# Optimization experiments

Hardware: AMD Instinct MI355X
Metric: run time of the kernel (lower is better)

The kernel has to match this reference:

```python
import jax, jax.numpy as jnp
import numpy as np

N = 100000
E = 1600000
G = 2048          # number of graphs in the batch
HEADS = 4
HID = 16          # per-head channels
IN_CH = 128
D = HEADS * HID   # 64, concat output width per layer
NEG_SLOPE = 0.2


def _gat_layer(x, src, dst, W, a_src, a_dst, bias):
    # x: [N, Fin], W: [Fin, H*C], a_src/a_dst: [H, C], bias: [H*C]
    h = (x @ W).reshape(N, HEADS, HID)                      # [N, H, C]
    al_s = jnp.einsum('nhc,hc->nh', h, a_src)               # [N, H]
    al_d = jnp.einsum('nhc,hc->nh', h, a_dst)               # [N, H]
    e = jax.nn.leaky_relu(al_s[src] + al_d[dst], NEG_SLOPE) # [E+N, H]
    # segment softmax over incoming edges of each destination node
    m = jax.ops.segment_max(e, dst, num_segments=N)         # [N, H]
    e = jnp.exp(e - m[dst])
    s = jax.ops.segment_sum(e, dst, num_segments=N)
    alpha = e / (s[dst] + 1e-16)                            # [E+N, H]
    msg = h[src] * alpha[..., None]                         # [E+N, H, C]
    out = jax.ops.segment_sum(msg, dst, num_segments=N)     # [N, H, C]
    return out.reshape(N, D) + bias


def setup_inputs() -> dict:
    key = jax.random.key(0)
    ks = jax.random.split(key, 16)
    x = jax.random.normal(ks[0], (N, IN_CH), dtype=jnp.float32)
    edge_index = jax.random.randint(ks[1], (2, E), 0, N, dtype=jnp.int64)
    batch = jnp.sort(jax.random.randint(ks[2], (N,), 0, G, dtype=jnp.int64))
    inp = {'x': x, 'edge_index': edge_index, 'batch': batch}
    fins = [IN_CH, D, D]
    for i, fin in enumerate(fins):
        kk = jax.random.split(ks[3 + i], 4)
        sc = 1.0 / np.sqrt(fin)
        inp[f'W{i}'] = jax.random.normal(kk[0], (fin, D), dtype=jnp.float32) * sc
        inp[f'as{i}'] = jax.random.normal(kk[1], (HEADS, HID), dtype=jnp.float32) * 0.1
        inp[f'ad{i}'] = jax.random.normal(kk[2], (HEADS, HID), dtype=jnp.float32) * 0.1
        inp[f'b{i}'] = jnp.zeros((D,), dtype=jnp.float32)
    inp['head_w'] = jax.random.normal(ks[10], (1, D), dtype=jnp.float32) * (1.0 / np.sqrt(D))
    inp['head_b'] = jnp.zeros((1,), dtype=jnp.float32)
    return inp


def reference(x, edge_index, batch,
              W0, as0, ad0, b0,
              W1, as1, ad1, b1,
              W2, as2, ad2, b2,
              head_w, head_b):
    # PyG GATConv adds self-loops by default
    loops = jnp.arange(N, dtype=edge_index.dtype)
    src = jnp.concatenate([edge_index[0], loops])
    dst = jnp.concatenate([edge_index[1], loops])
    layers = [(W0, as0, ad0, b0), (W1, as1, ad1, b1), (W2, as2, ad2, b2)]
    h = x.astype(jnp.float32)
    for (W, a_s, a_d, b) in layers:
        h = _gat_layer(h, src, dst, W, a_s, a_d, b)
        h = jax.nn.relu(h)  # dropout p=0.0 -> identity
    pooled = jax.ops.segment_sum(h, batch, num_segments=G)  # [G, D]
    out = pooled @ head_w.T + head_b                         # [G, 1]
    return out.reshape(-1)                                   # out_dim == 1 -> flatten
```

## Files before the change

### kernel.cpp

```cpp
#include <hip/hip_runtime.h>
#include <hip/hip_bf16.h>
#include <hip/hip_fp16.h>
#include <cstdint>
#include <cstddef>

#define NN 100000
#define EE 1600000
#define GG 2048

constexpr int NB_SCAN = (NN + 255) / 256;

__device__ __forceinline__ float lrelu(float v) { return v > 0.f ? v : 0.2f * v; }

__global__ void k_count(const int* __restrict__ ei, int* __restrict__ deg,
                        int* __restrict__ rank) {
    int i = blockIdx.x * blockDim.x + threadIdx.x;
    if (i >= EE + NN) return;
    int d = (i < EE) ? ei[EE + i] : (i - EE);
    rank[i] = atomicAdd(&deg[d], 1);
}

__global__ void k_scan1(const int* __restrict__ deg, int* __restrict__ offs,
                        int* __restrict__ bsums) {
    __shared__ int tmp[256];
    int tid = threadIdx.x;
    int i = blockIdx.x * 256 + tid;
    int v = (i < NN) ? deg[i] : 0;
    tmp[tid] = v; __syncthreads();
    for (int off = 1; off < 256; off <<= 1) {
        int t = (tid >= off) ? tmp[tid - off] : 0;
        __syncthreads();
        tmp[tid] += t;
        __syncthreads();
    }
    if (i < NN) offs[i] = tmp[tid] - v;
    if (tid == 255) bsums[blockIdx.x] = tmp[255];
}

__global__ void k_scan2(int* __restrict__ bsums) {
    __shared__ int tmp[512];
    int tid = threadIdx.x;
    int v = (tid < NB_SCAN) ? bsums[tid] : 0;
    tmp[tid] = v; __syncthreads();
    for (int off = 1; off < 512; off <<= 1) {
        int t = (tid >= off) ? tmp[tid - off] : 0;
        __syncthreads();
        tmp[tid] += t;
        __syncthreads();
    }
    if (tid < NB_SCAN) bsums[tid] = tmp[tid] - v;
}

__global__ void k_scan3(int* __restrict__ offs, const int* __restrict__ bsums) {
    int i = blockIdx.x * 256 + threadIdx.x;
    if (i < NN) offs[i] += bsums[blockIdx.x];
}

__global__ void k_scatter(const int* __restrict__ ei, const int* __restrict__ offs,
                          const int* __restrict__ rank, int* __restrict__ col) {
    int i = blockIdx.x * blockDim.x + threadIdx.x;
    if (i >= EE + NN) return;
    int s, d;
    if (i < EE) { s = ei[i]; d = ei[EE + i]; } else { s = d = i - EE; }
    col[offs[d] + rank[i]] = s;
}

template <int FIN>
__global__ __launch_bounds__(256) void k_gemm(const float* __restrict__ X,
                                              const float* __restrict__ W,
                                              const float* __restrict__ asrc,
                                              const float* __restrict__ adst,
                                              float* __restrict__ H,
                                              float* __restrict__ als,
                                              float* __restrict__ ald) {
    int j  = threadIdx.x & 63;
    int ty = threadIdx.x >> 6;
    int row = __builtin_amdgcn_readfirstlane(blockIdx.x * 16 + ty * 4);
    const float* x0 = X + (size_t)row * FIN;
    const float* x1 = x0 + FIN;
    const float* x2 = x1 + FIN;
    const float* x3 = x2 + FIN;
    float a0 = 0.f, a1 = 0.f, a2 = 0.f, a3 = 0.f;
#pragma unroll
    for (int k = 0; k < FIN; k += 4) {
        float4 xa = *(const float4*)(x0 + k);
        float4 xb = *(const float4*)(x1 + k);
        float4 xc = *(const float4*)(x2 + k);
        float4 xd = *(const float4*)(x3 + k);
        float w0 = W[(k + 0) * 64 + j];
        float w1 = W[(k + 1) * 64 + j];
        float w2 = W[(k + 2) * 64 + j];
        float w3 = W[(k + 3) * 64 + j];
        a0 += xa.x * w0 + xa.y * w1 + xa.z * w2 + xa.w * w3;
        a1 += xb.x * w0 + xb.y * w1 + xb.z * w2 + xb.w * w3;
        a2 += xc.x * w0 + xc.y * w1 + xc.z * w2 + xc.w * w3;
        a3 += xd.x * w0 + xd.y * w1 + xd.z * w2 + xd.w * w3;
    }
    H[(size_t)(row + 0) * 64 + j] = a0;
    H[(size_t)(row + 1) * 64 + j] = a1;
    H[(size_t)(row + 2) * 64 + j] = a2;
    H[(size_t)(row + 3) * 64 + j] = a3;
    float asj = asrc[j], adj = adst[j];
    float accs[4] = {a0, a1, a2, a3};
#pragma unroll
    for (int r = 0; r < 4; r++) {
        float vs = accs[r] * asj;
        float vd = accs[r] * adj;
#pragma unroll
        for (int off = 8; off > 0; off >>= 1) {
            vs += __shfl_xor(vs, off, 64);
            vd += __shfl_xor(vd, off, 64);
        }
        if ((j & 15) == 0) {
            int h = j >> 4;
            als[(size_t)(row + r) * 4 + h] = vs;
            ald[(size_t)(row + r) * 4 + h] = vd;
        }
    }
}

#define LWPITCH 260
__global__ __launch_bounds__(256) void k_agg(
    const float* __restrict__ H, const float* __restrict__ als,
    const float* __restrict__ ald, const int* __restrict__ offs,
    const int* __restrict__ deg, const int* __restrict__ col,
    const float* __restrict__ bias, float* __restrict__ Hout,
    const int* __restrict__ batch, const float* __restrict__ hw,
    float* __restrict__ out, int last) {
    __shared__ float lws[16 * LWPITCH];
    __shared__ int   lsi[16][64];
    int tid = threadIdx.x;
    int g = tid >> 4;
    int l = tid & 15;
    int n = blockIdx.x * 16 + g;
    int start = offs[n];
    int len = deg[n];
    float4 ad4 = ((const float4*)ald)[n];
    int hsel = l >> 2;
    const float4* Hp = (const float4*)H + l;
    float* lw = lws + g * LWPITCH;
    bool fast = (len <= 64);
    float inv = 1.f;

    if (fast) {
        float ev[4][4];
        int   si[4];
        bool  vld[4];
        float m0 = -1e30f, m1 = -1e30f, m2 = -1e30f, m3 = -1e30f;
#pragma unroll
        for (int it = 0; it < 4; it++) {
            int e = l + it * 16;
            vld[it] = (e < len);
            int s = vld[it] ? col[start + e] : 0;
            si[it] = s;
            float4 a = ((const float4*)als)[s];
            ev[it][0] = lrelu(a.x + ad4.x); ev[it][1] = lrelu(a.y + ad4.y);
            ev[it][2] = lrelu(a.z + ad4.z); ev[it][3] = lrelu(a.w + ad4.w);
            if (vld[it]) {
                m0 = fmaxf(m0, ev[it][0]); m1 = fmaxf(m1, ev[it][1]);
                m2 = fmaxf(m2, ev[it][2]); m3 = fmaxf(m3, ev[it][3]);
            }
        }
#pragma unroll
        for (int off = 8; off > 0; off >>= 1) {
            m0 = fmaxf(m0, __shfl_xor(m0, off, 16));
            m1 = fmaxf(m1, __shfl_xor(m1, off, 16));
            m2 = fmaxf(m2, __shfl_xor(m2, off, 16));
            m3 = fmaxf(m3, __shfl_xor(m3, off, 16));
        }
        float s0 = 0.f, s1 = 0.f, s2 = 0.f, s3 = 0.f;
#pragma unroll
        for (int it = 0; it < 4; it++) {
            int e = l + it * 16;
            float w0 = vld[it] ? __expf(ev[it][0] - m0) : 0.f;
            float w1 = vld[it] ? __expf(ev[it][1] - m1) : 0.f;
            float w2 = vld[it] ? __expf(ev[it][2] - m2) : 0.f;
            float w3 = vld[it] ? __expf(ev[it][3] - m3) : 0.f;
            s0 += w0; s1 += w1; s2 += w2; s3 += w3;
            ((float4*)(lw + e * 4))[0] = make_float4(w0, w1, w2, w3);
            lsi[g][e] = vld[it] ? si[it] : 0;
        }
#pragma unroll
        for (int off = 8; off > 0; off >>= 1) {
            s0 += __shfl_xor(s0, off, 16); s1 += __shfl_xor(s1, off, 16);
            s2 += __shfl_xor(s2, off, 16); s3 += __shfl_xor(s3, off, 16);
        }
        float smh = hsel == 0 ? s0 : hsel == 1 ? s1 : hsel == 2 ? s2 : s3;
        inv = 1.f / (smh + 1e-16f);
    }

    __syncthreads();

    float4 acc = {0.f, 0.f, 0.f, 0.f};
    if (fast) {
        int e = 0;
        for (; e + 4 <= len; e += 4) {
            int sa = lsi[g][e], sb = lsi[g][e + 1], sc = lsi[g][e + 2], sd = lsi[g][e + 3];
            float wa = lw[(e + 0) * 4 + hsel];
            float wb = lw[(e + 1) * 4 + hsel];
            float wc = lw[(e + 2) * 4 + hsel];
            float wd = lw[(e + 3) * 4 + hsel];
            float4 ha = Hp[(size_t)sa * 16];
            float4 hb = Hp[(size_t)sb * 16];
            float4 hc = Hp[(size_t)sc * 16];
            float4 hd = Hp[(size_t)sd * 16];
            acc.x += wa * ha.x + wb * hb.x + wc * hc.x + wd * hd.x;
            acc.y += wa * ha.y + wb * hb.y + wc * hc.y + wd * hd.y;
            acc.z += wa * ha.z + wb * hb.z + wc * hc.z + wd * hd.z;
            acc.w += wa * ha.w + wb * hb.w + wc * hc.w + wd * hd.w;
        }
        for (; e < len; e++) {
            int sa = lsi[g][e];
            float wa = lw[e * 4 + hsel];
            float4 ha = Hp[(size_t)sa * 16];
            acc.x += wa * ha.x; acc.y += wa * ha.y;
            acc.z += wa * ha.z; acc.w += wa * ha.w;
        }
    } else {
        float m0 = -1e30f, m1 = -1e30f, m2 = -1e30f, m3 = -1e30f;
        for (int e = l; e < len; e += 16) {
            int s = col[start + e];
            float4 a = ((const float4*)als)[s];
            m0 = fmaxf(m0, lrelu(a.x + ad4.x)); m1 = fmaxf(m1, lrelu(a.y + ad4.y));
            m2 = fmaxf(m2, lrelu(a.z + ad4.z)); m3 = fmaxf(m3, lrelu(a.w + ad4.w));
        }
#pragma unroll
        for (int off = 8; off > 0; off >>= 1) {
            m0 = fmaxf(m0, __shfl_xor(m0, off, 16));
            m1 = fmaxf(m1, __shfl_xor(m1, off, 16));
            m2 = fmaxf(m2, __shfl_xor(m2, off, 16));
            m3 = fmaxf(m3, __shfl_xor(m3, off, 16));
        }
        float s0 = 0.f, s1 = 0.f, s2 = 0.f, s3 = 0.f;
        for (int e = l; e < len; e += 16) {
            int s = col[start + e];
            float4 a = ((const float4*)als)[s];
            s0 += __expf(lrelu(a.x + ad4.x) - m0); s1 += __expf(lrelu(a.y + ad4.y) - m1);
            s2 += __expf(lrelu(a.z + ad4.z) - m2); s3 += __expf(lrelu(a.w + ad4.w) - m3);
        }
#pragma unroll
        for (int off = 8; off > 0; off >>= 1) {
            s0 += __shfl_xor(s0, off, 16); s1 += __shfl_xor(s1, off, 16);
            s2 += __shfl_xor(s2, off, 16); s3 += __shfl_xor(s3, off, 16);
        }
        float mh = hsel == 0 ? m0 : hsel == 1 ? m1 : hsel == 2 ? m2 : m3;
        float sh = hsel == 0 ? s0 : hsel == 1 ? s1 : hsel == 2 ? s2 : s3;
        float ih = 1.f / (sh + 1e-16f);
        float ah = hsel == 0 ? ad4.x : hsel == 1 ? ad4.y : hsel == 2 ? ad4.z : ad4.w;
        for (int e = 0; e < len; e++) {
            int s = col[start + e];
            float alpha = __expf(lrelu(als[(size_t)s * 4 + hsel] + ah) - mh) * ih;
            float4 ha = Hp[(size_t)s * 16];
            acc.x += alpha * ha.x; acc.y += alpha * ha.y;
            acc.z += alpha * ha.z; acc.w += alpha * ha.w;
        }
        inv = 1.f;
    }

    float4 b4 = ((const float4*)bias)[l];
    float4 o4;
    o4.x = fmaxf(acc.x * inv + b4.x, 0.f);
    o4.y = fmaxf(acc.y * inv + b4.y, 0.f);
    o4.z = fmaxf(acc.z * inv + b4.z, 0.f);
    o4.w = fmaxf(acc.w * inv + b4.w, 0.f);
    if (!last) {
        ((float4*)Hout)[(size_t)n * 16 + l] = o4;
    } else {
        float4 w4 = ((const float4*)hw)[l];
        float t = o4.x * w4.x + o4.y * w4.y + o4.z * w4.z + o4.w * w4.w;
#pragma unroll
        for (int off = 8; off > 0; off >>= 1) t += __shfl_xor(t, off, 16);
        if (l == 0) atomicAdd(&out[batch[n]], t);
    }
}

__global__ void k_out_init(const float* __restrict__ head_b, float* __restrict__ out) {
    int g = blockIdx.x * blockDim.x + threadIdx.x;
    if (g < GG) out[g] = head_b[0];
}

extern "C" void kernel_launch(void* const* d_in, const int* in_sizes, int n_in,
                              void* d_out, int out_size, void* d_ws, size_t ws_size,
                              hipStream_t stream) {
    const float* x     = (const float*)d_in[0];
    const int*   ei    = (const int*)d_in[1];
    const int*   batch = (const int*)d_in[2];
    const float* Wm[3] = {(const float*)d_in[3], (const float*)d_in[7],  (const float*)d_in[11]};
    const float* As[3] = {(const float*)d_in[4], (const float*)d_in[8],  (const float*)d_in[12]};
    const float* Ad[3] = {(const float*)d_in[5], (const float*)d_in[9],  (const float*)d_in[13]};
    const float* Bb[3] = {(const float*)d_in[6], (const float*)d_in[10], (const float*)d_in[14]};
    const float* hw = (const float*)d_in[15];
    const float* hb = (const float*)d_in[16];
    float* out = (float*)d_out;

    uint8_t* w = (uint8_t*)d_ws;
    auto alloc = [&](size_t bytes) -> void* {
        void* p = (void*)w;
        w += (bytes + 255) & ~(size_t)255;
        return p;
    };
    float* H       = (float*)alloc((size_t)NN * 64 * 4);
    float* Bf      = (float*)alloc((size_t)NN * 64 * 4);
    float* als     = (float*)alloc((size_t)NN * 4 * 4);
    float* ald     = (float*)alloc((size_t)NN * 4 * 4);
    int*   deg     = (int*)alloc((size_t)NN * 4);
    int*   offs    = (int*)alloc((size_t)NN * 4);
    int*   rank    = (int*)alloc((size_t)(EE + NN) * 4);
    int*   col     = (int*)alloc((size_t)(EE + NN) * 4);
    int*   bsums   = (int*)alloc((size_t)((NB_SCAN + 63) & ~63) * 4);

    hipMemsetAsync(deg, 0, (size_t)NN * 4, stream);

    int eb = (EE + NN + 255) / 256;
    k_count  <<<eb, 256, 0, stream>>>(ei, deg, rank);
    k_scan1  <<<NB_SCAN, 256, 0, stream>>>(deg, offs, bsums);
    k_scan2  <<<1, 512, 0, stream>>>(bsums);
    k_scan3  <<<NB_SCAN, 256, 0, stream>>>(offs, bsums);
    k_scatter<<<eb, 256, 0, stream>>>(ei, offs, rank, col);
    k_out_init<<<(GG + 255) / 256, 256, 0, stream>>>(hb, out);

    const float* cur_in = x;
    for (int L = 0; L < 3; L++) {
        if (L == 0)
            k_gemm<128><<<NN / 16, 256, 0, stream>>>(
                cur_in, Wm[L], As[L], Ad[L], H, als, ald);
        else
            k_gemm<64><<<NN / 16, 256, 0, stream>>>(
                cur_in, Wm[L], As[L], Ad[L], H, als, ald);
        k_agg <<<NN / 16, 256, 0, stream>>>(
            H, als, ald, offs, deg, col, Bb[L], Bf, batch, hw, out, (L == 2) ? 1 : 0);
        cur_in = Bf;
    }
}
```

Measured before the change: 540.5 us.

## Split aggregation into alpha pass and channel-sliced gather over planar H

The fused per-node aggregation is replaced by two kernels. The first computes normalized attention weights per edge and head into a head-major buffer. The second gathers from a feature matrix stored as 8 planes of 8 channels, so each pass touches a smaller, more cache-resident slice of H. Pooling moves to a separate kernel after the last layer. This adds an extra edge-sized alpha write and read per layer and re-reads the column indices 8 times, in exchange for better L2 locality in the gathers.

```diff
diff --git a/kernel.cpp b/kernel.cpp
--- a/kernel.cpp
+++ b/kernel.cpp
@@ -1,12 +1,12 @@
 #include <hip/hip_runtime.h>
 #include <hip/hip_bf16.h>
-#include <hip/hip_fp16.h>
 #include <cstdint>
 #include <cstddef>
 
 #define NN 100000
 #define EE 1600000
 #define GG 2048
+#define EN (EE + NN)
 
 constexpr int NB_SCAN = (NN + 255) / 256;
 
@@ -15,7 +15,7 @@
 __global__ void k_count(const int* __restrict__ ei, int* __restrict__ deg,
                         int* __restrict__ rank) {
     int i = blockIdx.x * blockDim.x + threadIdx.x;
-    if (i >= EE + NN) return;
+    if (i >= EN) return;
     int d = (i < EE) ? ei[EE + i] : (i - EE);
     rank[i] = atomicAdd(&deg[d], 1);
 }
@@ -59,7 +59,7 @@
 __global__ void k_scatter(const int* __restrict__ ei, const int* __restrict__ offs,
                           const int* __restrict__ rank, int* __restrict__ col) {
     int i = blockIdx.x * blockDim.x + threadIdx.x;
-    if (i >= EE + NN) return;
+    if (i >= EN) return;
     int s, d;
     if (i < EE) { s = ei[i]; d = ei[EE + i]; } else { s = d = i - EE; }
     col[offs[d] + rank[i]] = s;
@@ -70,7 +70,7 @@
                                               const float* __restrict__ W,
                                               const float* __restrict__ asrc,
                                               const float* __restrict__ adst,
-                                              float* __restrict__ H,
+                                              float* __restrict__ Hs,
                                               float* __restrict__ als,
                                               float* __restrict__ ald) {
     int j  = threadIdx.x & 63;
@@ -96,10 +96,9 @@
         a2 += xc.x * w0 + xc.y * w1 + xc.z * w2 + xc.w * w3;
         a3 += xd.x * w0 + xd.y * w1 + xd.z * w2 + xd.w * w3;
     }
-    H[(size_t)(row + 0) * 64 + j] = a0;
-    H[(size_t)(row + 1) * 64 + j] = a1;
-    H[(size_t)(row + 2) * 64 + j] = a2;
-    H[(size_t)(row + 3) * 64 + j] = a3;
+    int plane = j >> 3, cc = j & 7;
+    float* pb = Hs + ((size_t)plane * NN + row) * 8 + cc;
+    pb[0 * 8] = a0; pb[1 * 8] = a1; pb[2 * 8] = a2; pb[3 * 8] = a3;
     float asj = asrc[j], adj = adst[j];
     float accs[4] = {a0, a1, a2, a3};
 #pragma unroll
@@ -119,32 +118,19 @@
     }
 }
 
-#define LWPITCH 260
-__global__ __launch_bounds__(256) void k_agg(
-    const float* __restrict__ H, const float* __restrict__ als,
-    const float* __restrict__ ald, const int* __restrict__ offs,
-    const int* __restrict__ deg, const int* __restrict__ col,
-    const float* __restrict__ bias, float* __restrict__ Hout,
-    const int* __restrict__ batch, const float* __restrict__ hw,
-    float* __restrict__ out, int last) {
-    __shared__ float lws[16 * LWPITCH];
-    __shared__ int   lsi[16][64];
+__global__ __launch_bounds__(256) void k_alpha(
+    const float* __restrict__ als, const float* __restrict__ ald,
+    const int* __restrict__ offs, const int* __restrict__ deg,
+    const int* __restrict__ col, float* __restrict__ alpha) {
     int tid = threadIdx.x;
-    int g = tid >> 4;
-    int l = tid & 15;
+    int g = tid >> 4, l = tid & 15;
     int n = blockIdx.x * 16 + g;
     int start = offs[n];
     int len = deg[n];
     float4 ad4 = ((const float4*)ald)[n];
-    int hsel = l >> 2;
-    const float4* Hp = (const float4*)H + l;
-    float* lw = lws + g * LWPITCH;
-    bool fast = (len <= 64);
-    float inv = 1.f;
-
-    if (fast) {
+
+    if (len <= 64) {
         float ev[4][4];
-        int   si[4];
         bool  vld[4];
         float m0 = -1e30f, m1 = -1e30f, m2 = -1e30f, m3 = -1e30f;
 #pragma unroll
@@ -152,7 +138,6 @@
             int e = l + it * 16;
             vld[it] = (e < len);
             int s = vld[it] ? col[start + e] : 0;
-            si[it] = s;
             float4 a = ((const float4*)als)[s];
             ev[it][0] = lrelu(a.x + ad4.x); ev[it][1] = lrelu(a.y + ad4.y);
             ev[it][2] = lrelu(a.z + ad4.z); ev[it][3] = lrelu(a.w + ad4.w);
@@ -168,53 +153,32 @@
             m2 = fmaxf(m2, __shfl_xor(m2, off, 16));
             m3 = fmaxf(m3, __shfl_xor(m3, off, 16));
         }
+        float w[4][4];
         float s0 = 0.f, s1 = 0.f, s2 = 0.f, s3 = 0.f;
+#pragma unroll
+        for (int it = 0; it < 4; it++) {
+            w[it][0] = vld[it] ? __expf(ev[it][0] - m0) : 0.f;
+            w[it][1] = vld[it] ? __expf(ev[it][1] - m1) : 0.f;
+            w[it][2] = vld[it] ? __expf(ev[it][2] - m2) : 0.f;
+            w[it][3] = vld[it] ? __expf(ev[it][3] - m3) : 0.f;
+            s0 += w[it][0]; s1 += w[it][1]; s2 += w[it][2]; s3 += w[it][3];
+        }
+#pragma unroll
+        for (int off = 8; off > 0; off >>= 1) {
+            s0 += __shfl_xor(s0, off, 16); s1 += __shfl_xor(s1, off, 16);
+            s2 += __shfl_xor(s2, off, 16); s3 += __shfl_xor(s3, off, 16);
+        }
+        float i0 = 1.f / (s0 + 1e-16f), i1 = 1.f / (s1 + 1e-16f);
+        float i2 = 1.f / (s2 + 1e-16f), i3 = 1.f / (s3 + 1e-16f);
 #pragma unroll
         for (int it = 0; it < 4; it++) {
             int e = l + it * 16;
-            float w0 = vld[it] ? __expf(ev[it][0] - m0) : 0.f;
-            float w1 = vld[it] ? __expf(ev[it][1] - m1) : 0.f;
-            float w2 = vld[it] ? __expf(ev[it][2] - m2) : 0.f;
-            float w3 = vld[it] ? __expf(ev[it][3] - m3) : 0.f;
-            s0 += w0; s1 += w1; s2 += w2; s3 += w3;
-            ((float4*)(lw + e * 4))[0] = make_float4(w0, w1, w2, w3);
-            lsi[g][e] = vld[it] ? si[it] : 0;
-        }
-#pragma unroll
-        for (int off = 8; off > 0; off >>= 1) {
-            s0 += __shfl_xor(s0, off, 16); s1 += __shfl_xor(s1, off, 16);
-            s2 += __shfl_xor(s2, off, 16); s3 += __shfl_xor(s3, off, 16);
-        }
-        float smh = hsel == 0 ? s0 : hsel == 1 ? s1 : hsel == 2 ? s2 : s3;
-        inv = 1.f / (smh + 1e-16f);
-    }
-
-    __syncthreads();
-
-    float4 acc = {0.f, 0.f, 0.f, 0.f};
-    if (fast) {
-        int e = 0;
-        for (; e + 4 <= len; e += 4) {
-            int sa = lsi[g][e], sb = lsi[g][e + 1], sc = lsi[g][e + 2], sd = lsi[g][e + 3];
-            float wa = lw[(e + 0) * 4 + hsel];
-            float wb = lw[(e + 1) * 4 + hsel];
-            float wc = lw[(e + 2) * 4 + hsel];
-            float wd = lw[(e + 3) * 4 + hsel];
-            float4 ha = Hp[(size_t)sa * 16];
-            float4 hb = Hp[(size_t)sb * 16];
-            float4 hc = Hp[(size_t)sc * 16];
-            float4 hd = Hp[(size_t)sd * 16];
-            acc.x += wa * ha.x + wb * hb.x + wc * hc.x + wd * hd.x;
-            acc.y += wa * ha.y + wb * hb.y + wc * hc.y + wd * hd.y;
-            acc.z += wa * ha.z + wb * hb.z + wc * hc.z + wd * hd.z;
-            acc.w += wa * ha.w + wb * hb.w + wc * hc.w + wd * hd.w;
-        }
-        for (; e < len; e++) {
-            int sa = lsi[g][e];
-            float wa = lw[e * 4 + hsel];
-            float4 ha = Hp[(size_t)sa * 16];
-            acc.x += wa * ha.x; acc.y += wa * ha.y;
-            acc.z += wa * ha.z; acc.w += wa * ha.w;
+            if (vld[it]) {
+                alpha[0 * (size_t)EN + start + e] = w[it][0] * i0;
+                alpha[1 * (size_t)EN + start + e] = w[it][1] * i1;
+                alpha[2 * (size_t)EN + start + e] = w[it][2] * i2;
+                alpha[3 * (size_t)EN + start + e] = w[it][3] * i3;
+            }
         }
     } else {
         float m0 = -1e30f, m1 = -1e30f, m2 = -1e30f, m3 = -1e30f;
@@ -243,40 +207,85 @@
             s0 += __shfl_xor(s0, off, 16); s1 += __shfl_xor(s1, off, 16);
             s2 += __shfl_xor(s2, off, 16); s3 += __shfl_xor(s3, off, 16);
         }
-        float mh = hsel == 0 ? m0 : hsel == 1 ? m1 : hsel == 2 ? m2 : m3;
-        float sh = hsel == 0 ? s0 : hsel == 1 ? s1 : hsel == 2 ? s2 : s3;
-        float ih = 1.f / (sh + 1e-16f);
-        float ah = hsel == 0 ? ad4.x : hsel == 1 ? ad4.y : hsel == 2 ? ad4.z : ad4.w;
-        for (int e = 0; e < len; e++) {
+        float i0 = 1.f / (s0 + 1e-16f), i1 = 1.f / (s1 + 1e-16f);
+        float i2 = 1.f / (s2 + 1e-16f), i3 = 1.f / (s3 + 1e-16f);
+        for (int e = l; e < len; e += 16) {
             int s = col[start + e];
-            float alpha = __expf(lrelu(als[(size_t)s * 4 + hsel] + ah) - mh) * ih;
-            float4 ha = Hp[(size_t)s * 16];
-            acc.x += alpha * ha.x; acc.y += alpha * ha.y;
-            acc.z += alpha * ha.z; acc.w += alpha * ha.w;
-        }
-        inv = 1.f;
-    }
-
-    float4 b4 = ((const float4*)bias)[l];
+            float4 a = ((const float4*)als)[s];
+            alpha[0 * (size_t)EN + start + e] = __expf(lrelu(a.x + ad4.x) - m0) * i0;
+            alpha[1 * (size_t)EN + start + e] = __expf(lrelu(a.y + ad4.y) - m1) * i1;
+            alpha[2 * (size_t)EN + start + e] = __expf(lrelu(a.z + ad4.z) - m2) * i2;
+            alpha[3 * (size_t)EN + start + e] = __expf(lrelu(a.w + ad4.w) - m3) * i3;
+        }
+    }
+}
+
+__global__ __launch_bounds__(256) void k_slice(
+    const float* __restrict__ Hs, const float* __restrict__ alpha,
+    const int* __restrict__ offs, const int* __restrict__ deg,
+    const int* __restrict__ col, const float* __restrict__ bias,
+    float* __restrict__ Hout) {
+    int s = blockIdx.x & 7;
+    int t = blockIdx.x >> 3;
+    int n = t * 128 + (threadIdx.x >> 1);
+    if (n >= NN) return;
+    int c  = threadIdx.x & 1;
+    int c4 = s * 2 + c;
+    int h  = c4 >> 2;
+    const float*  ap = alpha + (size_t)h * EN;
+    const float4* Hp = (const float4*)Hs + (size_t)s * NN * 2 + c;
+    int start = offs[n];
+    int len = deg[n];
+    const int*   cp  = col + start;
+    const float* app = ap + start;
+    float4 acc = {0.f, 0.f, 0.f, 0.f};
+    int e = 0;
+    for (; e + 4 <= len; e += 4) {
+        int i0 = cp[e], i1 = cp[e + 1], i2 = cp[e + 2], i3 = cp[e + 3];
+        float a0 = app[e], a1 = app[e + 1], a2 = app[e + 2], a3 = app[e + 3];
+        float4 h0 = Hp[(size_t)i0 * 2];
+        float4 h1 = Hp[(size_t)i1 * 2];
+        float4 h2 = Hp[(size_t)i2 * 2];
+        float4 h3 = Hp[(size_t)i3 * 2];
+        acc.x += a0 * h0.x + a1 * h1.x + a2 * h2.x + a3 * h3.x;
+        acc.y += a0 * h0.y + a1 * h1.y + a2 * h2.y + a3 * h3.y;
+        acc.z += a0 * h0.z + a1 * h1.z + a2 * h2.z + a3 * h3.z;
+        acc.w += a0 * h0.w + a1 * h1.w + a2 * h2.w + a3 * h3.w;
+    }
+    for (; e < len; e++) {
+        int i0 = cp[e];
+        float a0 = app[e];
+        float4 h0 = Hp[(size_t)i0 * 2];
+        acc.x += a0 * h0.x; acc.y += a0 * h0.y;
+        acc.z += a0 * h0.z; acc.w += a0 * h0.w;
+    }
+    float4 b4 = ((const float4*)bias)[c4];
     float4 o4;
-    o4.x = fmaxf(acc.x * inv + b4.x, 0.f);
-    o4.y = fmaxf(acc.y * inv + b4.y, 0.f);
-    o4.z = fmaxf(acc.z * inv + b4.z, 0.f);
-    o4.w = fmaxf(acc.w * inv + b4.w, 0.f);
-    if (!last) {
-        ((float4*)Hout)[(size_t)n * 16 + l] = o4;
-    } else {
-        float4 w4 = ((const float4*)hw)[l];
-        float t = o4.x * w4.x + o4.y * w4.y + o4.z * w4.z + o4.w * w4.w;
-#pragma unroll
-        for (int off = 8; off > 0; off >>= 1) t += __shfl_xor(t, off, 16);
-        if (l == 0) atomicAdd(&out[batch[n]], t);
-    }
+    o4.x = fmaxf(acc.x + b4.x, 0.f);
+    o4.y = fmaxf(acc.y + b4.y, 0.f);
+    o4.z = fmaxf(acc.z + b4.z, 0.f);
+    o4.w = fmaxf(acc.w + b4.w, 0.f);
+    ((float4*)Hout)[(size_t)n * 16 + c4] = o4;
 }
 
 __global__ void k_out_init(const float* __restrict__ head_b, float* __restrict__ out) {
     int g = blockIdx.x * blockDim.x + threadIdx.x;
     if (g < GG) out[g] = head_b[0];
+}
+
+__global__ void k_pool(const float* __restrict__ H, const int* __restrict__ batch,
+                       const float* __restrict__ hw, float* __restrict__ out) {
+    int n = blockIdx.x * blockDim.x + threadIdx.x;
+    if (n >= NN) return;
+    const float4* hp = (const float4*)(H + (size_t)n * 64);
+    const float4* wp = (const float4*)hw;
+    float t = 0.f;
+#pragma unroll
+    for (int k = 0; k < 16; k++) {
+        float4 a = hp[k]; float4 b = wp[k];
+        t += a.x * b.x + a.y * b.y + a.z * b.z + a.w * b.w;
+    }
+    atomicAdd(&out[batch[n]], t);
 }
 
 extern "C" void kernel_launch(void* const* d_in, const int* in_sizes, int n_in,
@@ -299,19 +308,20 @@
         w += (bytes + 255) & ~(size_t)255;
         return p;
     };
-    float* H       = (float*)alloc((size_t)NN * 64 * 4);
-    float* Bf      = (float*)alloc((size_t)NN * 64 * 4);
-    float* als     = (float*)alloc((size_t)NN * 4 * 4);
-    float* ald     = (float*)alloc((size_t)NN * 4 * 4);
-    int*   deg     = (int*)alloc((size_t)NN * 4);
-    int*   offs    = (int*)alloc((size_t)NN * 4);
-    int*   rank    = (int*)alloc((size_t)(EE + NN) * 4);
-    int*   col     = (int*)alloc((size_t)(EE + NN) * 4);
-    int*   bsums   = (int*)alloc((size_t)((NB_SCAN + 63) & ~63) * 4);
+    float* Hs    = (float*)alloc((size_t)8 * NN * 8 * 4);
+    float* Bf    = (float*)alloc((size_t)NN * 64 * 4);
+    float* als   = (float*)alloc((size_t)NN * 4 * 4);
+    float* ald   = (float*)alloc((size_t)NN * 4 * 4);
+    int*   deg   = (int*)alloc((size_t)NN * 4);
+    int*   offs  = (int*)alloc((size_t)NN * 4);
+    int*   col   = (int*)alloc((size_t)EN * 4);
+    float* alpha = (float*)alloc((size_t)4 * EN * 4);
+    int*   bsums = (int*)alloc((size_t)((NB_SCAN + 63) & ~63) * 4);
+    int*   rank  = (int*)alpha;
 
     hipMemsetAsync(deg, 0, (size_t)NN * 4, stream);
 
-    int eb = (EE + NN + 255) / 256;
+    int eb = (EN + 255) / 256;
     k_count  <<<eb, 256, 0, stream>>>(ei, deg, rank);
     k_scan1  <<<NB_SCAN, 256, 0, stream>>>(deg, offs, bsums);
     k_scan2  <<<1, 512, 0, stream>>>(bsums);
@@ -319,16 +329,18 @@
     k_scatter<<<eb, 256, 0, stream>>>(ei, offs, rank, col);
     k_out_init<<<(GG + 255) / 256, 256, 0, stream>>>(hb, out);
 
+    int slice_blocks = ((NN + 127) / 128) * 8;
     const float* cur_in = x;
     for (int L = 0; L < 3; L++) {
         if (L == 0)
             k_gemm<128><<<NN / 16, 256, 0, stream>>>(
-                cur_in, Wm[L], As[L], Ad[L], H, als, ald);
+                cur_in, Wm[L], As[L], Ad[L], Hs, als, ald);
         else
             k_gemm<64><<<NN / 16, 256, 0, stream>>>(
-                cur_in, Wm[L], As[L], Ad[L], H, als, ald);
-        k_agg <<<NN / 16, 256, 0, stream>>>(
-            H, als, ald, offs, deg, col, Bb[L], Bf, batch, hw, out, (L == 2) ? 1 : 0);
+                cur_in, Wm[L], As[L], Ad[L], Hs, als, ald);
+        k_alpha<<<NN / 16, 256, 0, stream>>>(als, ald, offs, deg, col, alpha);
+        k_slice<<<slice_blocks, 256, 0, stream>>>(Hs, alpha, offs, deg, col, Bb[L], Bf);
         cur_in = Bf;
     }
-}
+    k_pool<<<(NN + 255) / 256, 256, 0, stream>>>(Bf, batch, hw, out);
+}
```

Result: slower. 809.4 us (+49.8%).
